# Optimization experiments

Measured on AMD Instinct MI355X. Metric: run time of the kernel, lower is better.

Reference implementation:

```python
import jax, jax.numpy as jnp
import numpy as np

D = 1024  # bilinear_dim
IN_A = 1024
IN_B = 1024

def setup_inputs() -> dict:
    key = jax.random.key(0)
    ks = jax.random.split(key, 8)
    B, La, Lb = 64, 256, 256
    sa = 1.0 / np.sqrt(IN_A)
    sb = 1.0 / np.sqrt(IN_B)
    sd = 1.0 / np.sqrt(D)
    return {
        "a": jax.random.normal(ks[0], (B, La, IN_A), dtype=jnp.float32),
        "b": jax.random.normal(ks[1], (B, Lb, IN_B), dtype=jnp.float32),
        "Wa": jax.random.uniform(ks[2], (IN_A, D), jnp.float32, -sa, sa),
        "ba": jax.random.uniform(ks[3], (D,), jnp.float32, -sa, sa),
        "Wb": jax.random.uniform(ks[4], (IN_B, D), jnp.float32, -sb, sb),
        "bb": jax.random.uniform(ks[5], (D,), jnp.float32, -sb, sb),
        "w": jax.random.uniform(ks[6], (D,), jnp.float32, -sd, sd),
        "wbias": jax.random.uniform(ks[7], (), jnp.float32, -sd, sd),
    }

def reference(a, b, Wa, ba, Wb, bb, w, wbias):
    # Linear projections (dropout inactive at inference)
    pa = a @ Wa + ba          # (B, La, D)
    pb = b @ Wb + bb          # (B, Lb, D)
    # Fused bilinear score: sum_d w[d]*pa[b,i,d]*pb[b,j,d] + wbias
    # (equivalent to materializing (B,La,Lb,D) outer product then Linear(D->1))
    scores = jnp.einsum('bid,bjd->bij', pa * w, pb) + wbias  # (B, La, Lb)
    B, La, Lb = scores.shape
    norm = jax.nn.softmax(scores.reshape(B, La * Lb), axis=1)
    return norm.reshape(B, La, Lb)
```

## Files before the change

### kernel.cpp

```cpp
#include <hip/hip_runtime.h>
#include <hip/hip_bf16.h>

typedef __attribute__((ext_vector_type(8))) short bf16x8;
typedef __attribute__((ext_vector_type(4))) float f32x4;

#define K_DIM 1024
#define M_PROJ 16384
#define NBATCH 64
#define SEQ 256

static __device__ inline unsigned short bf16_bits(float f) {
    __hip_bfloat16 h = __float2bfloat16(f);
    return *reinterpret_cast<unsigned short*>(&h);
}

#define GLOAD16(g, l) __builtin_amdgcn_global_load_lds(                          \
    (__attribute__((address_space(1))) void*)(g),                                \
    (__attribute__((address_space(3))) void*)(l), 16, 0, 0)

__global__ __launch_bounds__(256) void prep(const float* __restrict__ Wa,
                                            const float* __restrict__ Wb,
                                            const float* __restrict__ w,
                                            const float* __restrict__ ba,
                                            const float* __restrict__ bb,
                                            unsigned short* __restrict__ Waw,
                                            unsigned short* __restrict__ Wb16,
                                            float* __restrict__ u,
                                            float* __restrict__ v,
                                            float* __restrict__ c)
{
    const int blk = blockIdx.x;
    const int t = threadIdx.x;
    if (blk < 1024) {
        const int scale_by_w = (blk < 512);
        const float* in = scale_by_w ? Wa : Wb;
        unsigned short* out = scale_by_w ? Waw : Wb16;
        const int i = (scale_by_w ? blk : blk - 512) * 256 + t;
        const int d0 = (i * 8) & (K_DIM - 1);
        const float4* p = reinterpret_cast<const float4*>(in) + (size_t)i * 2;
        float4 v0 = p[0], v1 = p[1];
        if (scale_by_w) {
            float4 w0 = *(const float4*)&w[d0];
            float4 w1 = *(const float4*)&w[d0 + 4];
            v0.x *= w0.x; v0.y *= w0.y; v0.z *= w0.z; v0.w *= w0.w;
            v1.x *= w1.x; v1.y *= w1.y; v1.z *= w1.z; v1.w *= w1.w;
        }
        unsigned short uo[8];
        uo[0] = bf16_bits(v0.x); uo[1] = bf16_bits(v0.y); uo[2] = bf16_bits(v0.z); uo[3] = bf16_bits(v0.w);
        uo[4] = bf16_bits(v1.x); uo[5] = bf16_bits(v1.y); uo[6] = bf16_bits(v1.z); uo[7] = bf16_bits(v1.w);
        *reinterpret_cast<uint4*>(out + (size_t)i * 8) = *reinterpret_cast<uint4*>(uo);
        return;
    }
    __shared__ float psum[4];
    const int p = blk - 1024;
    const int d0 = t * 4;
    float part = 0.f;
    if (p < 1024) {
        float4 m = *(const float4*)&Wa[(size_t)p * K_DIM + d0];
        float4 ww = *(const float4*)&w[d0];
        float4 bv = *(const float4*)&bb[d0];
        part = m.x * ww.x * bv.x + m.y * ww.y * bv.y + m.z * ww.z * bv.z + m.w * ww.w * bv.w;
    } else if (p < 2048) {
        float4 m = *(const float4*)&Wb[(size_t)(p - 1024) * K_DIM + d0];
        float4 ww = *(const float4*)&w[d0];
        float4 bv = *(const float4*)&ba[d0];
        part = m.x * ww.x * bv.x + m.y * ww.y * bv.y + m.z * ww.z * bv.z + m.w * ww.w * bv.w;
    } else {
        float4 ww = *(const float4*)&w[d0];
        float4 b1 = *(const float4*)&ba[d0];
        float4 b2 = *(const float4*)&bb[d0];
        part = ww.x * b1.x * b2.x + ww.y * b1.y * b2.y + ww.z * b1.z * b2.z + ww.w * b1.w * b2.w;
    }
#pragma unroll
    for (int off = 32; off; off >>= 1) part += __shfl_down(part, off);
    if ((t & 63) == 0) psum[t >> 6] = part;
    __syncthreads();
    if (t == 0) {
        const float s = (psum[0] + psum[1]) + (psum[2] + psum[3]);
        if (p < 1024) u[p] = s;
        else if (p < 2048) v[p - 1024] = s;
        else *c = s;
    }
}

__global__ __launch_bounds__(256) void conv_rows(const float* __restrict__ X,
                                                 const float* __restrict__ dvec,
                                                 unsigned short* __restrict__ out,
                                                 float* __restrict__ rowdot)
{
    __shared__ float psum[4];
    const int t = threadIdx.x;
    const int r = blockIdx.x * 2 + (t >> 7);
    const int c8 = (t & 127) * 8;

    const float* xp = &X[(size_t)r * K_DIM + c8];
    float4 v0 = *(const float4*)xp;
    float4 v1 = *(const float4*)(xp + 4);
    float4 u0 = *(const float4*)&dvec[c8];
    float4 u1 = *(const float4*)&dvec[c8 + 4];
    float part = v0.x * u0.x + v0.y * u0.y + v0.z * u0.z + v0.w * u0.w
               + v1.x * u1.x + v1.y * u1.y + v1.z * u1.z + v1.w * u1.w;

    unsigned short uo[8];
    uo[0] = bf16_bits(v0.x); uo[1] = bf16_bits(v0.y); uo[2] = bf16_bits(v0.z); uo[3] = bf16_bits(v0.w);
    uo[4] = bf16_bits(v1.x); uo[5] = bf16_bits(v1.y); uo[6] = bf16_bits(v1.z); uo[7] = bf16_bits(v1.w);
    *reinterpret_cast<uint4*>(&out[(size_t)r * K_DIM + c8]) = *reinterpret_cast<uint4*>(uo);

#pragma unroll
    for (int off = 32; off; off >>= 1) part += __shfl_down(part, off);
    if ((t & 63) == 0) psum[t >> 6] = part;
    __syncthreads();
    if ((t & 127) == 0) rowdot[r] = psum[(t >> 6)] + psum[(t >> 6) + 1];
}

__global__ __launch_bounds__(256) void mt_gemm(const __hip_bfloat16* __restrict__ Wb16,
                                               const __hip_bfloat16* __restrict__ Waw,
                                               unsigned short* __restrict__ Mt)
{
    __shared__ __align__(16) unsigned short As[128][32];
    __shared__ __align__(16) unsigned short Bs[128][32];

    const int tid  = threadIdx.x;
    const int lane = tid & 63;
    const int wave = tid >> 6;
    const int q0 = blockIdx.x * 128;
    const int p0 = blockIdx.y * 128;
    const int wr = (wave >> 1) * 64;
    const int wc = (wave & 1) * 64;

    const __hip_bfloat16* Arow = Wb16 + (size_t)q0 * K_DIM;
    const __hip_bfloat16* Brow = Waw + (size_t)p0 * K_DIM;

    f32x4 acc[4][4];
#pragma unroll
    for (int i = 0; i < 4; ++i)
#pragma unroll
        for (int j = 0; j < 4; ++j) acc[i][j] = f32x4{0.f, 0.f, 0.f, 0.f};

    const int lrow = lane & 15;
    const int kq   = (lane >> 4) * 8;

    for (int k0 = 0; k0 < K_DIM; k0 += 32) {
        __syncthreads();
#pragma unroll
        for (int it = 0; it < 2; ++it) {
            const int chunk = (it * 4 + wave) * 64 + lane;
            const int row = chunk >> 2;
            const int col = (chunk & 3) * 8;
            GLOAD16(Arow + (size_t)row * K_DIM + k0 + col,
                    reinterpret_cast<char*>(&As[0][0]) + (it * 4 + wave) * 1024);
        }
#pragma unroll
        for (int it = 0; it < 2; ++it) {
            const int chunk = (it * 4 + wave) * 64 + lane;
            const int row = chunk >> 2;
            const int col = (chunk & 3) * 8;
            GLOAD16(Brow + (size_t)row * K_DIM + k0 + col,
                    reinterpret_cast<char*>(&Bs[0][0]) + (it * 4 + wave) * 1024);
        }
        __syncthreads();

        bf16x8 af[4], bfr[4];
#pragma unroll
        for (int f = 0; f < 4; ++f) {
            af[f]  = *reinterpret_cast<const bf16x8*>(&As[wr + f * 16 + lrow][kq]);
            bfr[f] = *reinterpret_cast<const bf16x8*>(&Bs[wc + f * 16 + lrow][kq]);
        }
#pragma unroll
        for (int i = 0; i < 4; ++i)
#pragma unroll
            for (int j = 0; j < 4; ++j)
                acc[i][j] = __builtin_amdgcn_mfma_f32_16x16x32_bf16(bfr[j], af[i], acc[i][j], 0, 0, 0);
    }

#pragma unroll
    for (int ii = 0; ii < 4; ++ii) {
        const int q = q0 + wr + ii * 16 + lrow;
#pragma unroll
        for (int jj = 0; jj < 4; ++jj) {
            const int pb = p0 + wc + jj * 16 + (lane >> 4) * 4;
            unsigned short uo[4];
            uo[0] = bf16_bits(acc[ii][jj][0]);
            uo[1] = bf16_bits(acc[ii][jj][1]);
            uo[2] = bf16_bits(acc[ii][jj][2]);
            uo[3] = bf16_bits(acc[ii][jj][3]);
            *(ushort4*)&Mt[(size_t)q * K_DIM + pb] = *(ushort4*)uo;
        }
    }
}

__global__ __launch_bounds__(512, 2) void proj_gemm256(
    const __hip_bfloat16* __restrict__ A,
    const __hip_bfloat16* __restrict__ Wt,
    const float* __restrict__ bias,
    const float* __restrict__ scale,
    __hip_bfloat16* __restrict__ out,
    int use_bias, int use_scale)
{
    __shared__ __align__(16) unsigned short lds[2][4][128 * 64];

    const int tid  = threadIdx.x;
    const int lane = tid & 63;
    const int w    = tid >> 6;
    const int wr   = w >> 2;
    const int wc   = w & 3;
    const int m0 = blockIdx.x * 256;
    const int n0 = blockIdx.y * 256;

    const int c1 = w * 128 + lane, c2 = c1 + 64;
    const int r1 = c1 >> 3, r2 = c2 >> 3;
    const int k1 = (c1 & 7) ^ (r1 & 7);
    const int k2 = (c2 & 7) ^ (r2 & 7);

    const int lrow = lane & 15;
    const int kq0  = (((lane >> 4) + 0) ^ (lane & 7)) * 16;
    const int kq1  = (((lane >> 4) + 4) ^ (lane & 7)) * 16;

#define STG(SRC, RB, KB, BUF, REG)                                               \
    {                                                                            \
        GLOAD16((SRC) + (size_t)((RB) + r1) * K_DIM + (KB) + k1 * 8,             \
                (char*)(&lds[BUF][REG][0]) + w * 2048);                          \
        GLOAD16((SRC) + (size_t)((RB) + r2) * K_DIM + (KB) + k2 * 8,             \
                (char*)(&lds[BUF][REG][0]) + w * 2048 + 1024);                   \
    }

    f32x4 acc[8][4];
#pragma unroll
    for (int i = 0; i < 8; ++i)
#pragma unroll
        for (int j = 0; j < 4; ++j) acc[i][j] = f32x4{0.f, 0.f, 0.f, 0.f};

    STG(A,  m0,       0, 0, 0); STG(A,  m0 + 128,  0, 0, 1);
    STG(Wt, n0,       0, 0, 2); STG(Wt, n0 + 128,  0, 0, 3);
    STG(A,  m0,      64, 1, 0); STG(A,  m0 + 128, 64, 1, 1);
    asm volatile("s_waitcnt vmcnt(4)" ::: "memory");
    __builtin_amdgcn_sched_barrier(0);
    __builtin_amdgcn_s_barrier();

#define KTILE(CUR, NXT, T)                                                       \
    {                                                                            \
        const int kb1 = (((T) + 1) & 15) << 6;                                   \
        const int kb2 = (((T) + 2) & 15) << 6;                                   \
        const char* Ab = (const char*)(&lds[CUR][wr][0]);                        \
        const char* Bb = (const char*)(&lds[CUR][2 + (wc >> 1)][0])              \
                         + (wc & 1) * 8192;                                      \
        bf16x8 af[4][2], bfr[4][2];                                              \
        _Pragma("unroll")                                                        \
        for (int mi = 0; mi < 4; ++mi) {                                         \
            af[mi][0] = *(const bf16x8*)(Ab + mi * 2048 + lrow * 128 + kq0);     \
            af[mi][1] = *(const bf16x8*)(Ab + mi * 2048 + lrow * 128 + kq1);     \
        }                                                                        \
        _Pragma("unroll")                                                        \
        for (int nj = 0; nj < 2; ++nj) {                                         \
            bfr[nj][0] = *(const bf16x8*)(Bb + nj * 2048 + lrow * 128 + kq0);    \
            bfr[nj][1] = *(const bf16x8*)(Bb + nj * 2048 + lrow * 128 + kq1);    \
        }                                                                        \
        STG(Wt, n0, kb1, NXT, 2);                                                \
        __builtin_amdgcn_sched_barrier(0);                                       \
        __builtin_amdgcn_s_barrier();                                            \
        asm volatile("s_waitcnt lgkmcnt(0)" ::: "memory");                       \
        __builtin_amdgcn_sched_barrier(0);                                       \
        __builtin_amdgcn_s_setprio(1);                                           \
        _Pragma("unroll")                                                        \
        for (int mi = 0; mi < 4; ++mi)                                           \
            _Pragma("unroll")                                                    \
            for (int nj = 0; nj < 2; ++nj) {                                     \
                acc[mi][nj] = __builtin_amdgcn_mfma_f32_16x16x32_bf16(           \
                    bfr[nj][0], af[mi][0], acc[mi][nj], 0, 0, 0);                \
                acc[mi][nj] = __builtin_amdgcn_mfma_f32_16x16x32_bf16(           \
                    bfr[nj][1], af[mi][1], acc[mi][nj], 0, 0, 0);                \
            }                                                                    \
        __builtin_amdgcn_s_setprio(0);                                           \
        __builtin_amdgcn_sched_barrier(0);                                       \
        __builtin_amdgcn_s_barrier();                                            \
        _Pragma("unroll")                                                        \
        for (int nj = 2; nj < 4; ++nj) {                                         \
            bfr[nj][0] = *(const bf16x8*)(Bb + nj * 2048 + lrow * 128 + kq0);    \
            bfr[nj][1] = *(const bf16x8*)(Bb + nj * 2048 + lrow * 128 + kq1);    \
        }                                                                        \
        STG(Wt, n0 + 128, kb1, NXT, 3);                                          \
        __builtin_amdgcn_sched_barrier(0);                                       \
        __builtin_amdgcn_s_barrier();                                            \
        asm volatile("s_waitcnt lgkmcnt(0)" ::: "memory");                       \
        __builtin_amdgcn_sched_barrier(0);                                       \
        __builtin_amdgcn_s_setprio(1);                                           \
        _Pragma("unroll")                                                        \
        for (int mi = 0; mi < 4; ++mi)                                           \
            _Pragma("unroll")                                                    \
            for (int nj = 2; nj < 4; ++nj) {                                     \
                acc[mi][nj] = __builtin_amdgcn_mfma_f32_16x16x32_bf16(           \
                    bfr[nj][0], af[mi][0], acc[mi][nj], 0, 0, 0);                \
                acc[mi][nj] = __builtin_amdgcn_mfma_f32_16x16x32_bf16(           \
                    bfr[nj][1], af[mi][1], acc[mi][nj], 0, 0, 0);                \
            }                                                                    \
        __builtin_amdgcn_s_setprio(0);                                           \
        __builtin_amdgcn_sched_barrier(0);                                       \
        __builtin_amdgcn_s_barrier();                                            \
        _Pragma("unroll")                                                        \
        for (int mi = 0; mi < 4; ++mi) {                                         \
            af[mi][0] = *(const bf16x8*)(Ab + 8192 + mi * 2048 + lrow * 128 + kq0);\
            af[mi][1] = *(const bf16x8*)(Ab + 8192 + mi * 2048 + lrow * 128 + kq1);\
        }                                                                        \
        __builtin_amdgcn_sched_barrier(0);                                       \
        __builtin_amdgcn_s_barrier();                                            \
        asm volatile("s_waitcnt lgkmcnt(0)" ::: "memory");                       \
        __builtin_amdgcn_sched_barrier(0);                                       \
        __builtin_amdgcn_s_setprio(1);                                           \
        _Pragma("unroll")                                                        \
        for (int mi = 0; mi < 4; ++mi)                                           \
            _Pragma("unroll")                                                    \
            for (int nj = 0; nj < 2; ++nj) {                                     \
                acc[4 + mi][nj] = __builtin_amdgcn_mfma_f32_16x16x32_bf16(       \
                    bfr[nj][0], af[mi][0], acc[4 + mi][nj], 0, 0, 0);            \
                acc[4 + mi][nj] = __builtin_amdgcn_mfma_f32_16x16x32_bf16(       \
                    bfr[nj][1], af[mi][1], acc[4 + mi][nj], 0, 0, 0);            \
            }                                                                    \
        __builtin_amdgcn_s_setprio(0);                                           \
        __builtin_amdgcn_sched_barrier(0);                                       \
        __builtin_amdgcn_s_barrier();                                            \
        STG(A, m0,       kb2, CUR, 0);                                           \
        STG(A, m0 + 128, kb2, CUR, 1);                                           \
        __builtin_amdgcn_sched_barrier(0);                                       \
        __builtin_amdgcn_s_barrier();                                            \
        __builtin_amdgcn_s_setprio(1);                                           \
        _Pragma("unroll")                                                        \
        for (int mi = 0; mi < 4; ++mi)                                           \
            _Pragma("unroll")                                                    \
            for (int nj = 2; nj < 4; ++nj) {                                     \
                acc[4 + mi][nj] = __builtin_amdgcn_mfma_f32_16x16x32_bf16(       \
                    bfr[nj][0], af[mi][0], acc[4 + mi][nj], 0, 0, 0);            \
                acc[4 + mi][nj] = __builtin_amdgcn_mfma_f32_16x16x32_bf16(       \
                    bfr[nj][1], af[mi][1], acc[4 + mi][nj], 0, 0, 0);            \
            }                                                                    \
        __builtin_amdgcn_s_setprio(0);                                           \
        asm volatile("s_waitcnt vmcnt(4)" ::: "memory");                         \
        __builtin_amdgcn_sched_barrier(0);                                       \
        __builtin_amdgcn_s_barrier();                                            \
    }

    for (int tt = 0; tt < 8; ++tt) {
        const int t0 = tt * 2;
        KTILE(0, 1, t0);
        KTILE(1, 0, t0 + 1);
    }
#undef KTILE
#undef STG

    asm volatile("s_waitcnt vmcnt(0)" ::: "memory");
    __builtin_amdgcn_sched_barrier(0);
    __builtin_amdgcn_s_barrier();
    char* eb = (char*)(&lds[0][0][0]);
#pragma unroll
    for (int mi8 = 0; mi8 < 8; ++mi8) {
        const int ml = wr * 128 + (mi8 >> 2) * 64 + (mi8 & 3) * 16 + lrow;
#pragma unroll
        for (int nj = 0; nj < 4; ++nj) {
            const int nl = wc * 64 + nj * 16 + (lane >> 4) * 4;
            const int nb = n0 + nl;
            float4 bc = float4{0.f, 0.f, 0.f, 0.f};
            float4 sc = float4{1.f, 1.f, 1.f, 1.f};
            if (use_bias)  bc = *(const float4*)&bias[nb];
            if (use_scale) sc = *(const float4*)&scale[nb];
            unsigned short uo[4];
            uo[0] = bf16_bits((acc[mi8][nj][0] + bc.x) * sc.x);
            uo[1] = bf16_bits((acc[mi8][nj][1] + bc.y) * sc.y);
            uo[2] = bf16_bits((acc[mi8][nj][2] + bc.z) * sc.z);
            uo[3] = bf16_bits((acc[mi8][nj][3] + bc.w) * sc.w);
            const int v = nl >> 3;
            *(ushort4*)(eb + ml * 512 + ((v ^ (ml & 7)) * 16) + ((nl >> 2) & 1) * 8)
                = *(ushort4*)uo;
        }
    }
    __syncthreads();
#pragma unroll
    for (int p = 0; p < 2; ++p) {
        const int ml = p * 128 + (tid >> 2);
#pragma unroll
        for (int it = 0; it < 8; ++it) {
            const int v = it * 4 + (tid & 3);
            uint4 val = *(const uint4*)(eb + ml * 512 + ((v ^ (ml & 7)) * 16));
            *(uint4*)&out[(size_t)(m0 + ml) * K_DIM + n0 + v * 8] = val;
        }
    }
}

__global__ __launch_bounds__(256) void score_gemm(const __hip_bfloat16* __restrict__ T,
                                                  const __hip_bfloat16* __restrict__ Bbf,
                                                  const float* __restrict__ alpha,
                                                  const float* __restrict__ beta,
                                                  const float* __restrict__ cptr,
                                                  const float* __restrict__ wbias,
                                                  float* __restrict__ out,
                                                  float* __restrict__ partials)
{
    __shared__ __align__(16) unsigned short As[128][32];
    __shared__ __align__(16) unsigned short Bs[128][32];
    __shared__ float psum[4];

    const int tid  = threadIdx.x;
    const int lane = tid & 63;
    const int wave = tid >> 6;
    const int b  = blockIdx.z;
    const int i0 = blockIdx.x * 128;
    const int j0 = blockIdx.y * 128;
    const int wr = (wave >> 1) * 64;
    const int wc = (wave & 1) * 64;

    const __hip_bfloat16* Arow = T + (size_t)(b * SEQ + i0) * K_DIM;
    const __hip_bfloat16* Brow = Bbf + (size_t)(b * SEQ + j0) * K_DIM;

    f32x4 acc[4][4];
#pragma unroll
    for (int i = 0; i < 4; ++i)
#pragma unroll
        for (int j = 0; j < 4; ++j) acc[i][j] = f32x4{0.f, 0.f, 0.f, 0.f};

    const int lrow = lane & 15;
    const int kq   = (lane >> 4) * 8;

    for (int k0 = 0; k0 < K_DIM; k0 += 32) {
        __syncthreads();
#pragma unroll
        for (int it = 0; it < 2; ++it) {
            const int chunk = (it * 4 + wave) * 64 + lane;
            const int row = chunk >> 2;
            const int col = (chunk & 3) * 8;
            GLOAD16(Arow + (size_t)row * K_DIM + k0 + col,
                    reinterpret_cast<char*>(&As[0][0]) + (it * 4 + wave) * 1024);
        }
#pragma unroll
        for (int it = 0; it < 2; ++it) {
            const int chunk = (it * 4 + wave) * 64 + lane;
            const int row = chunk >> 2;
            const int col = (chunk & 3) * 8;
            GLOAD16(Brow + (size_t)row * K_DIM + k0 + col,
                    reinterpret_cast<char*>(&Bs[0][0]) + (it * 4 + wave) * 1024);
        }
        __syncthreads();

        bf16x8 af[4], bfr[4];
#pragma unroll
        for (int f = 0; f < 4; ++f) {
            af[f]  = *reinterpret_cast<const bf16x8*>(&As[wr + f * 16 + lrow][kq]);
            bfr[f] = *reinterpret_cast<const bf16x8*>(&Bs[wc + f * 16 + lrow][kq]);
        }
#pragma unroll
        for (int i = 0; i < 4; ++i)
#pragma unroll
            for (int j = 0; j < 4; ++j)
                acc[i][j] = __builtin_amdgcn_mfma_f32_16x16x32_bf16(bfr[j], af[i], acc[i][j], 0, 0, 0);
    }

    const float cwb = *cptr + *wbias;
    float lsum = 0.f;
#pragma unroll
    for (int ii = 0; ii < 4; ++ii) {
        const int i = i0 + wr + ii * 16 + lrow;
        const float av = alpha[b * SEQ + i] + cwb;
#pragma unroll
        for (int jj = 0; jj < 4; ++jj) {
            const int jb = j0 + wc + jj * 16 + (lane >> 4) * 4;
            const float4 bv = *(const float4*)&beta[b * SEQ + jb];
            float4 e;
            e.x = __expf(acc[ii][jj][0] + av + bv.x);
            e.y = __expf(acc[ii][jj][1] + av + bv.y);
            e.z = __expf(acc[ii][jj][2] + av + bv.z);
            e.w = __expf(acc[ii][jj][3] + av + bv.w);
            lsum += (e.x + e.y) + (e.z + e.w);
            *(float4*)&out[(size_t)b * (SEQ * SEQ) + (size_t)i * SEQ + jb] = e;
        }
    }
#pragma unroll
    for (int off = 32; off; off >>= 1) lsum += __shfl_down(lsum, off);
    if (lane == 0) psum[wave] = lsum;
    __syncthreads();
    if (tid == 0)
        partials[b * 4 + blockIdx.x * 2 + blockIdx.y] =
            (psum[0] + psum[1]) + (psum[2] + psum[3]);
}

__global__ __launch_bounds__(1024) void normalize_k(float* __restrict__ s,
                                                    const float* __restrict__ partials)
{
    const int b    = blockIdx.x >> 2;
    const int part = blockIdx.x & 3;
    const float inv = 1.0f / (((partials[b * 4 + 0] + partials[b * 4 + 1]) +
                               partials[b * 4 + 2]) + partials[b * 4 + 3]);
    float4* p4 = reinterpret_cast<float4*>(s + (size_t)b * (SEQ * SEQ));
    const int base = part * 4096;
#pragma unroll
    for (int it = 0; it < 4; ++it) {
        const int i = base + it * 1024 + threadIdx.x;
        float4 v = p4[i];
        v.x *= inv; v.y *= inv; v.z *= inv; v.w *= inv;
        p4[i] = v;
    }
}

extern "C" void kernel_launch(void* const* d_in, const int* in_sizes, int n_in,
                              void* d_out, int out_size, void* d_ws, size_t ws_size,
                              hipStream_t stream)
{
    const float* a     = (const float*)d_in[0];
    const float* b     = (const float*)d_in[1];
    const float* Wa    = (const float*)d_in[2];
    const float* ba    = (const float*)d_in[3];
    const float* Wb    = (const float*)d_in[4];
    const float* bb    = (const float*)d_in[5];
    const float* w     = (const float*)d_in[6];
    const float* wbias = (const float*)d_in[7];
    float* out = (float*)d_out;

    char* wsb = (char*)d_ws;
    unsigned short* Waw   = (unsigned short*)(wsb);
    unsigned short* Wb16  = (unsigned short*)(wsb + (size_t)2097152);
    unsigned short* Mt    = (unsigned short*)(wsb + (size_t)4194304);
    float* u              = (float*)(wsb + (size_t)6291456);
    float* v              = (float*)(wsb + (size_t)6291456 + 4096);
    float* c              = (float*)(wsb + (size_t)6291456 + 8192);
    float* alpha          = (float*)(wsb + (size_t)6291456 + 16384);
    float* beta           = (float*)(wsb + (size_t)6291456 + 16384 + 65536);
    float* partials       = (float*)(wsb + (size_t)6291456 + 16384 + 131072);
    unsigned short* ab16  = (unsigned short*)(wsb + (size_t)8388608);
    unsigned short* Tbuf  = (unsigned short*)(wsb + (size_t)41943040);

    prep<<<3073, 256, 0, stream>>>(Wa, Wb, w, ba, bb, Waw, Wb16, u, v, c);
    mt_gemm<<<dim3(8, 8), 256, 0, stream>>>((const __hip_bfloat16*)Wb16,
                                            (const __hip_bfloat16*)Waw, Mt);
    conv_rows<<<M_PROJ / 2, 256, 0, stream>>>(a, u, ab16, alpha);
    const dim3 pgrid(M_PROJ / 256, K_DIM / 256);
    proj_gemm256<<<pgrid, 512, 0, stream>>>((const __hip_bfloat16*)ab16,
                                            (const __hip_bfloat16*)Mt,
                                            u, u, (__hip_bfloat16*)Tbuf, 0, 0);
    conv_rows<<<M_PROJ / 2, 256, 0, stream>>>(b, v, ab16, beta);
    const dim3 sgrid(SEQ / 128, SEQ / 128, NBATCH);
    score_gemm<<<sgrid, 256, 0, stream>>>((const __hip_bfloat16*)Tbuf,
                                          (const __hip_bfloat16*)ab16,
                                          alpha, beta, c, wbias, out, partials);
    normalize_k<<<NBATCH * 4, 1024, 0, stream>>>(out, partials);
}
```

Before: 128.9 us.

## Fuse softmax normalization into score GEMM via per-batch atomic sync; fold u/v into prep

The score GEMM keeps its exponentiated tile in registers and publishes its partial sum with a release store. It then bumps a per-batch atomic counter and spins until all four tiles of that batch have arrived, and scales and writes the output once. This removes the separate normalize kernel's extra read and write of the full 16 MB output. The prep kernel now computes the u/v row dot products during the weight bf16 conversion pass instead of re-reading Wa/Wb in 2048 extra blocks, and it resets the counters. The spin-wait relies on all blocks of a batch being co-resident, which holds for this 256-block grid but is a deadlock risk in general.

Result: no change. 130.2 us (+1.1%).

```diff
diff --git a/kernel.cpp b/kernel.cpp
--- a/kernel.cpp
+++ b/kernel.cpp
@@ -27,60 +27,68 @@
                                             unsigned short* __restrict__ Wb16,
                                             float* __restrict__ u,
                                             float* __restrict__ v,
-                                            float* __restrict__ c)
+                                            float* __restrict__ c,
+                                            unsigned int* __restrict__ counters)
 {
+    __shared__ float psum[4];
     const int blk = blockIdx.x;
     const int t = threadIdx.x;
+
     if (blk < 1024) {
-        const int scale_by_w = (blk < 512);
-        const float* in = scale_by_w ? Wa : Wb;
-        unsigned short* out = scale_by_w ? Waw : Wb16;
-        const int i = (scale_by_w ? blk : blk - 512) * 256 + t;
-        const int d0 = (i * 8) & (K_DIM - 1);
-        const float4* p = reinterpret_cast<const float4*>(in) + (size_t)i * 2;
-        float4 v0 = p[0], v1 = p[1];
-        if (scale_by_w) {
-            float4 w0 = *(const float4*)&w[d0];
-            float4 w1 = *(const float4*)&w[d0 + 4];
+        const int isA = (blk < 512);
+        const int r  = (isA ? blk : blk - 512) * 2 + (t >> 7);
+        const int c8 = (t & 127) * 8;
+        const float* in  = isA ? Wa : Wb;
+        const float* bv  = isA ? bb : ba;
+        unsigned short* o = isA ? Waw : Wb16;
+
+        const float* xp = &in[(size_t)r * K_DIM + c8];
+        float4 v0 = *(const float4*)xp;
+        float4 v1 = *(const float4*)(xp + 4);
+        float4 w0 = *(const float4*)&w[c8];
+        float4 w1 = *(const float4*)&w[c8 + 4];
+        float4 b0 = *(const float4*)&bv[c8];
+        float4 b1 = *(const float4*)&bv[c8 + 4];
+
+        float part = v0.x * w0.x * b0.x + v0.y * w0.y * b0.y
+                   + v0.z * w0.z * b0.z + v0.w * w0.w * b0.w
+                   + v1.x * w1.x * b1.x + v1.y * w1.y * b1.y
+                   + v1.z * w1.z * b1.z + v1.w * w1.w * b1.w;
+
+        if (isA) {
             v0.x *= w0.x; v0.y *= w0.y; v0.z *= w0.z; v0.w *= w0.w;
             v1.x *= w1.x; v1.y *= w1.y; v1.z *= w1.z; v1.w *= w1.w;
         }
         unsigned short uo[8];
         uo[0] = bf16_bits(v0.x); uo[1] = bf16_bits(v0.y); uo[2] = bf16_bits(v0.z); uo[3] = bf16_bits(v0.w);
         uo[4] = bf16_bits(v1.x); uo[5] = bf16_bits(v1.y); uo[6] = bf16_bits(v1.z); uo[7] = bf16_bits(v1.w);
-        *reinterpret_cast<uint4*>(out + (size_t)i * 8) = *reinterpret_cast<uint4*>(uo);
+        *reinterpret_cast<uint4*>(&o[(size_t)r * K_DIM + c8]) = *reinterpret_cast<uint4*>(uo);
+
+#pragma unroll
+        for (int off = 32; off; off >>= 1) part += __shfl_down(part, off);
+        if ((t & 63) == 0) psum[t >> 6] = part;
+        __syncthreads();
+        if ((t & 127) == 0) {
+            const float s = psum[t >> 6] + psum[(t >> 6) + 1];
+            if (isA) u[r] = s; else v[r] = s;
+        }
         return;
     }
-    __shared__ float psum[4];
-    const int p = blk - 1024;
+    if (blk == 1025) {
+        if (t < NBATCH) counters[t] = 0u;
+        return;
+    }
     const int d0 = t * 4;
-    float part = 0.f;
-    if (p < 1024) {
-        float4 m = *(const float4*)&Wa[(size_t)p * K_DIM + d0];
-        float4 ww = *(const float4*)&w[d0];
-        float4 bv = *(const float4*)&bb[d0];
-        part = m.x * ww.x * bv.x + m.y * ww.y * bv.y + m.z * ww.z * bv.z + m.w * ww.w * bv.w;
-    } else if (p < 2048) {
-        float4 m = *(const float4*)&Wb[(size_t)(p - 1024) * K_DIM + d0];
-        float4 ww = *(const float4*)&w[d0];
-        float4 bv = *(const float4*)&ba[d0];
-        part = m.x * ww.x * bv.x + m.y * ww.y * bv.y + m.z * ww.z * bv.z + m.w * ww.w * bv.w;
-    } else {
-        float4 ww = *(const float4*)&w[d0];
-        float4 b1 = *(const float4*)&ba[d0];
-        float4 b2 = *(const float4*)&bb[d0];
-        part = ww.x * b1.x * b2.x + ww.y * b1.y * b2.y + ww.z * b1.z * b2.z + ww.w * b1.w * b2.w;
-    }
+    float4 ww = *(const float4*)&w[d0];
+    float4 b1 = *(const float4*)&ba[d0];
+    float4 b2 = *(const float4*)&bb[d0];
+    float part = ww.x * b1.x * b2.x + ww.y * b1.y * b2.y
+               + ww.z * b1.z * b2.z + ww.w * b1.w * b2.w;
 #pragma unroll
     for (int off = 32; off; off >>= 1) part += __shfl_down(part, off);
     if ((t & 63) == 0) psum[t >> 6] = part;
     __syncthreads();
-    if (t == 0) {
-        const float s = (psum[0] + psum[1]) + (psum[2] + psum[3]);
-        if (p < 1024) u[p] = s;
-        else if (p < 2048) v[p - 1024] = s;
-        else *c = s;
-    }
+    if (t == 0) *c = (psum[0] + psum[1]) + (psum[2] + psum[3]);
 }
 
 __global__ __launch_bounds__(256) void conv_rows(const float* __restrict__ X,
@@ -192,10 +200,7 @@
 __global__ __launch_bounds__(512, 2) void proj_gemm256(
     const __hip_bfloat16* __restrict__ A,
     const __hip_bfloat16* __restrict__ Wt,
-    const float* __restrict__ bias,
-    const float* __restrict__ scale,
-    __hip_bfloat16* __restrict__ out,
-    int use_bias, int use_scale)
+    __hip_bfloat16* __restrict__ out)
 {
     __shared__ __align__(16) unsigned short lds[2][4][128 * 64];
 
@@ -356,18 +361,13 @@
 #pragma unroll
         for (int nj = 0; nj < 4; ++nj) {
             const int nl = wc * 64 + nj * 16 + (lane >> 4) * 4;
-            const int nb = n0 + nl;
-            float4 bc = float4{0.f, 0.f, 0.f, 0.f};
-            float4 sc = float4{1.f, 1.f, 1.f, 1.f};
-            if (use_bias)  bc = *(const float4*)&bias[nb];
-            if (use_scale) sc = *(const float4*)&scale[nb];
             unsigned short uo[4];
-            uo[0] = bf16_bits((acc[mi8][nj][0] + bc.x) * sc.x);
-            uo[1] = bf16_bits((acc[mi8][nj][1] + bc.y) * sc.y);
-            uo[2] = bf16_bits((acc[mi8][nj][2] + bc.z) * sc.z);
-            uo[3] = bf16_bits((acc[mi8][nj][3] + bc.w) * sc.w);
-            const int v = nl >> 3;
-            *(ushort4*)(eb + ml * 512 + ((v ^ (ml & 7)) * 16) + ((nl >> 2) & 1) * 8)
+            uo[0] = bf16_bits(acc[mi8][nj][0]);
+            uo[1] = bf16_bits(acc[mi8][nj][1]);
+            uo[2] = bf16_bits(acc[mi8][nj][2]);
+            uo[3] = bf16_bits(acc[mi8][nj][3]);
+            const int vv = nl >> 3;
+            *(ushort4*)(eb + ml * 512 + ((vv ^ (ml & 7)) * 16) + ((nl >> 2) & 1) * 8)
                 = *(ushort4*)uo;
         }
     }
@@ -377,9 +377,9 @@
         const int ml = p * 128 + (tid >> 2);
 #pragma unroll
         for (int it = 0; it < 8; ++it) {
-            const int v = it * 4 + (tid & 3);
-            uint4 val = *(const uint4*)(eb + ml * 512 + ((v ^ (ml & 7)) * 16));
-            *(uint4*)&out[(size_t)(m0 + ml) * K_DIM + n0 + v * 8] = val;
+            const int vv = it * 4 + (tid & 3);
+            uint4 val = *(const uint4*)(eb + ml * 512 + ((vv ^ (ml & 7)) * 16));
+            *(uint4*)&out[(size_t)(m0 + ml) * K_DIM + n0 + vv * 8] = val;
         }
     }
 }
@@ -391,11 +391,13 @@
                                                   const float* __restrict__ cptr,
                                                   const float* __restrict__ wbias,
                                                   float* __restrict__ out,
-                                                  float* __restrict__ partials)
+                                                  float* __restrict__ partials,
+                                                  unsigned int* __restrict__ counters)
 {
     __shared__ __align__(16) unsigned short As[128][32];
     __shared__ __align__(16) unsigned short Bs[128][32];
     __shared__ float psum[4];
+    __shared__ float inv_s;
 
     const int tid  = threadIdx.x;
     const int lane = tid & 63;
@@ -461,39 +463,46 @@
         for (int jj = 0; jj < 4; ++jj) {
             const int jb = j0 + wc + jj * 16 + (lane >> 4) * 4;
             const float4 bv = *(const float4*)&beta[b * SEQ + jb];
-            float4 e;
-            e.x = __expf(acc[ii][jj][0] + av + bv.x);
-            e.y = __expf(acc[ii][jj][1] + av + bv.y);
-            e.z = __expf(acc[ii][jj][2] + av + bv.z);
-            e.w = __expf(acc[ii][jj][3] + av + bv.w);
-            lsum += (e.x + e.y) + (e.z + e.w);
-            *(float4*)&out[(size_t)b * (SEQ * SEQ) + (size_t)i * SEQ + jb] = e;
+            acc[ii][jj][0] = __expf(acc[ii][jj][0] + av + bv.x);
+            acc[ii][jj][1] = __expf(acc[ii][jj][1] + av + bv.y);
+            acc[ii][jj][2] = __expf(acc[ii][jj][2] + av + bv.z);
+            acc[ii][jj][3] = __expf(acc[ii][jj][3] + av + bv.w);
+            lsum += (acc[ii][jj][0] + acc[ii][jj][1]) + (acc[ii][jj][2] + acc[ii][jj][3]);
         }
     }
 #pragma unroll
     for (int off = 32; off; off >>= 1) lsum += __shfl_down(lsum, off);
     if (lane == 0) psum[wave] = lsum;
     __syncthreads();
-    if (tid == 0)
-        partials[b * 4 + blockIdx.x * 2 + blockIdx.y] =
-            (psum[0] + psum[1]) + (psum[2] + psum[3]);
-}
-
-__global__ __launch_bounds__(1024) void normalize_k(float* __restrict__ s,
-                                                    const float* __restrict__ partials)
-{
-    const int b    = blockIdx.x >> 2;
-    const int part = blockIdx.x & 3;
-    const float inv = 1.0f / (((partials[b * 4 + 0] + partials[b * 4 + 1]) +
-                               partials[b * 4 + 2]) + partials[b * 4 + 3]);
-    float4* p4 = reinterpret_cast<float4*>(s + (size_t)b * (SEQ * SEQ));
-    const int base = part * 4096;
-#pragma unroll
-    for (int it = 0; it < 4; ++it) {
-        const int i = base + it * 1024 + threadIdx.x;
-        float4 v = p4[i];
-        v.x *= inv; v.y *= inv; v.z *= inv; v.w *= inv;
-        p4[i] = v;
+
+    const int pidx = b * 4 + blockIdx.x * 2 + blockIdx.y;
+    if (tid == 0) {
+        const float my = (psum[0] + psum[1]) + (psum[2] + psum[3]);
+        __hip_atomic_store(&partials[pidx], my, __ATOMIC_RELEASE, __HIP_MEMORY_SCOPE_AGENT);
+        __hip_atomic_fetch_add(&counters[b], 1u, __ATOMIC_RELEASE, __HIP_MEMORY_SCOPE_AGENT);
+        while (__hip_atomic_load(&counters[b], __ATOMIC_ACQUIRE, __HIP_MEMORY_SCOPE_AGENT) < 4u) {}
+        const float p0 = __hip_atomic_load(&partials[b * 4 + 0], __ATOMIC_RELAXED, __HIP_MEMORY_SCOPE_AGENT);
+        const float p1 = __hip_atomic_load(&partials[b * 4 + 1], __ATOMIC_RELAXED, __HIP_MEMORY_SCOPE_AGENT);
+        const float p2 = __hip_atomic_load(&partials[b * 4 + 2], __ATOMIC_RELAXED, __HIP_MEMORY_SCOPE_AGENT);
+        const float p3 = __hip_atomic_load(&partials[b * 4 + 3], __ATOMIC_RELAXED, __HIP_MEMORY_SCOPE_AGENT);
+        inv_s = 1.0f / (((p0 + p1) + p2) + p3);
+    }
+    __syncthreads();
+    const float inv = inv_s;
+
+#pragma unroll
+    for (int ii = 0; ii < 4; ++ii) {
+        const int i = i0 + wr + ii * 16 + lrow;
+#pragma unroll
+        for (int jj = 0; jj < 4; ++jj) {
+            const int jb = j0 + wc + jj * 16 + (lane >> 4) * 4;
+            float4 e;
+            e.x = acc[ii][jj][0] * inv;
+            e.y = acc[ii][jj][1] * inv;
+            e.z = acc[ii][jj][2] * inv;
+            e.w = acc[ii][jj][3] * inv;
+            *(float4*)&out[(size_t)b * (SEQ * SEQ) + (size_t)i * SEQ + jb] = e;
+        }
     }
 }
 
@@ -521,21 +530,21 @@
     float* alpha          = (float*)(wsb + (size_t)6291456 + 16384);
     float* beta           = (float*)(wsb + (size_t)6291456 + 16384 + 65536);
     float* partials       = (float*)(wsb + (size_t)6291456 + 16384 + 131072);
+    unsigned int* counters= (unsigned int*)(wsb + (size_t)6291456 + 16384 + 131072 + 1024);
     unsigned short* ab16  = (unsigned short*)(wsb + (size_t)8388608);
     unsigned short* Tbuf  = (unsigned short*)(wsb + (size_t)41943040);
 
-    prep<<<3073, 256, 0, stream>>>(Wa, Wb, w, ba, bb, Waw, Wb16, u, v, c);
+    prep<<<1026, 256, 0, stream>>>(Wa, Wb, w, ba, bb, Waw, Wb16, u, v, c, counters);
     mt_gemm<<<dim3(8, 8), 256, 0, stream>>>((const __hip_bfloat16*)Wb16,
                                             (const __hip_bfloat16*)Waw, Mt);
     conv_rows<<<M_PROJ / 2, 256, 0, stream>>>(a, u, ab16, alpha);
     const dim3 pgrid(M_PROJ / 256, K_DIM / 256);
     proj_gemm256<<<pgrid, 512, 0, stream>>>((const __hip_bfloat16*)ab16,
                                             (const __hip_bfloat16*)Mt,
-                                            u, u, (__hip_bfloat16*)Tbuf, 0, 0);
+                                            (__hip_bfloat16*)Tbuf);
     conv_rows<<<M_PROJ / 2, 256, 0, stream>>>(b, v, ab16, beta);
     const dim3 sgrid(SEQ / 128, SEQ / 128, NBATCH);
     score_gemm<<<sgrid, 256, 0, stream>>>((const __hip_bfloat16*)Tbuf,
                                           (const __hip_bfloat16*)ab16,
-                                          alpha, beta, c, wbias, out, partials);
-    normalize_k<<<NBATCH * 4, 1024, 0, stream>>>(out, partials);
-}
+                                          alpha, beta, c, wbias, out, partials, counters);
+}
```
